# Performance work log

Measured on AMD Instinct MI355X. Metric: run time of the kernel, lower is better.

Reference implementation:

```python
import jax, jax.numpy as jnp
import numpy as np

T, G, K, N = 131072, 64, 1024, 512  # batch_sum, batch_count, k, n
M_MAX = 4096  # static upper bound on any group size (setup guarantees <= 3072)
PAD = 128     # tile alignment for padded offsets


def setup_inputs() -> dict:
    key = jax.random.key(0)
    k1, k2 = jax.random.split(key)
    a = jax.random.normal(k1, (T, K), dtype=jnp.float32)
    b = jax.random.normal(k2, (G, K, N), dtype=jnp.float32) / np.float32(np.sqrt(K))
    rng = np.random.default_rng(0)
    d = rng.integers(-1024, 1024, G // 2)
    deltas = np.concatenate([d, -d])
    rng.shuffle(deltas)
    sizes = (T // G) + deltas  # each in [1024, 3072], sums exactly to T
    offsets = np.concatenate([[0], np.cumsum(sizes)[:-1]])
    padded = ((sizes + PAD - 1) // PAD) * PAD
    padded_offsets = np.concatenate([[0], np.cumsum(padded)[:-1]])
    return {
        "a": a,
        "b": b,
        "batch_sizes": jnp.asarray(sizes, dtype=jnp.int32),
        "batch_offsets": jnp.asarray(offsets, dtype=jnp.int32),
        "batch_padded_offsets": jnp.asarray(padded_offsets, dtype=jnp.int32),
    }


def reference(a, b, batch_sizes, batch_offsets, batch_padded_offsets):
    # Grouped GEMM: for each group g, out[off_g : off_g+size_g] = a[rows] @ b[g].
    # jit-friendly: scan over groups with a fixed M_MAX window, mask invalid rows.
    T_, _ = a.shape
    n_out = b.shape[-1]
    iota = jnp.arange(M_MAX)

    def body(out, xs):
        off, size, bg = xs
        rows = jnp.clip(off + iota, 0, T_ - 1)          # [M_MAX]
        mask = iota < size                               # [M_MAX]
        a_g = jnp.where(mask[:, None], a[rows], 0.0)     # [M_MAX, K]
        y = a_g @ bg                                     # [M_MAX, N]
        out = out.at[rows].add(y)                        # masked rows add zeros
        return out, None

    out0 = jnp.zeros((T_, n_out), dtype=a.dtype)
    out, _ = jax.lax.scan(body, out0, (batch_offsets, batch_sizes, b))
    return out
```

## Files before the change

kernel.cpp:

```cpp
#include <hip/hip_runtime.h>
#include <hip/hip_bf16.h>
#include <stdint.h>

#define T_ROWS 131072
#define GCNT   64
#define KDIM   1024
#define NDIM   512
#define BM     256
#define BN     256
#define BK     64
#define KTILES (KDIM / BK)
#define MT_MAX 640
#define NBLK   (MT_MAX * 2)

typedef __attribute__((ext_vector_type(4))) float f32x4;
typedef __attribute__((ext_vector_type(8))) short s16x8;
typedef __attribute__((ext_vector_type(4))) short s16x4;
typedef __attribute__((address_space(3))) unsigned int lds_u32;
typedef const __attribute__((address_space(1))) unsigned int gbl_u32;

static __device__ __forceinline__ short f2bf(float f) {
  __hip_bfloat16 h = __float2bfloat16(f);
  return __builtin_bit_cast(short, h);
}

__global__ __launch_bounds__(256) void bt_kernel(const float* __restrict__ b,
                                                 char* __restrict__ bt) {
  __shared__ short lt[64 * 130];
  int bid = blockIdx.x;
  int kt = bid & 15, nt = (bid >> 4) & 3, g = bid >> 6;
  int t = threadIdx.x;
  const float* src = b + ((size_t)(g * KDIM + kt * BK)) * NDIM + nt * 128;
#pragma unroll
  for (int i = 0; i < 32; i++) {
    int idx = i * 256 + t;
    int kk = idx >> 7, nn = idx & 127;
    lt[kk * 130 + nn] = f2bf(src[(size_t)kk * NDIM + nn]);
  }
  __syncthreads();
  char* dst = bt + ((size_t)bid << 14);
#pragma unroll
  for (int j = 0; j < 4; j++) {
    int chunk = j * 256 + t;
    int n = chunk >> 3;
    int slot = (chunk & 7) ^ (n & 7);
    s16x8 v;
#pragma unroll
    for (int i = 0; i < 8; i++) v[i] = lt[(slot * 8 + i) * 130 + n];
    *(s16x8*)(dst + (size_t)chunk * 16) = v;
  }
}

template <bool USE_BT>
__global__ __launch_bounds__(512, 2) void gemm_kernel(
    const float* __restrict__ a, const float* __restrict__ b,
    const char* __restrict__ bt, const int* __restrict__ sizes,
    const int* __restrict__ offs, float* __restrict__ out) {
  __shared__ __align__(16) short lds_a[2][BM * BK];
  __shared__ __align__(16) char lds_b[2][BN * BK * 2];

  int bid0 = blockIdx.x;
  int bid = (bid0 & 7) * (NBLK / 8) + (bid0 >> 3);
  int bn = bid & 1;
  int tm = bid >> 1;

  int g = -1, m_loc = 0, base = 0;
#pragma unroll
  for (int i = 0; i < GCNT; i++) {
    int ps = (sizes[i] + 127) & ~127;
    int tg = (ps + 255) >> 8;
    if (tm >= base && tm < base + tg) { g = i; m_loc = (tm - base) << 8; }
    base += tg;
  }
  if (g < 0) return;
  int size = sizes[g];
  int off = offs[g];
  int valid = size - m_loc;

  int t = threadIdx.x;
  int lane = t & 63;
  int wid = t >> 6;
  int wm = wid >> 2, wn = wid & 3;
  int lr = lane & 15, q = lane >> 4;

  int r0 = t >> 4;
  int c16 = t & 15;
  int aoff[8];
#pragma unroll
  for (int i = 0; i < 8; i++) {
    int row = off + m_loc + i * 32 + r0;
    if (row >= T_ROWS) row = T_ROWS - 1;
    aoff[i] = row * KDIM + c16 * 4;
  }
  int a_wbyte = r0 * 128 + (((c16 >> 1) ^ (r0 & 7)) << 4) + (c16 & 1) * 8;

  int fb_n = t >> 1, fb_kh = (t & 1) * 32;

  const char* btbase = bt + (((size_t)g) << 20);

  f32x4 acc[8][4];
#pragma unroll
  for (int i = 0; i < 8; i++)
#pragma unroll
    for (int j = 0; j < 4; j++) acc[i][j] = (f32x4){0.f, 0.f, 0.f, 0.f};

  f32x4 va[8];

  auto loadA = [&](int kt) {
#pragma unroll
    for (int i = 0; i < 8; i++)
      va[i] = *(const f32x4*)(a + aoff[i] + kt * BK);
  };
  auto writeA = [&](int c) {
    char* db = (char*)lds_a[c] + a_wbyte;
#pragma unroll
    for (int i = 0; i < 8; i++) {
      s16x4 v;
#pragma unroll
      for (int e = 0; e < 4; e++) v[e] = f2bf(va[i][e]);
      *(s16x4*)(db + i * 4096) = v;
    }
  };
  auto stageB_bt = [&](int kt, int c) {
#pragma unroll
    for (int i = 0; i < 4; i++) {
      int wc = wid * 4 + i;
      int sub = wc >> 4;
      int cc = (wc & 15) * 64 + lane;
      const char* gsrc =
          btbase + (((size_t)((bn * 2 + sub) * 16 + kt)) << 14) + cc * 16;
      __builtin_amdgcn_global_load_lds(
          (gbl_u32*)gsrc, (lds_u32*)((char*)lds_b[c] + wc * 1024), 16, 0, 0);
    }
  };
  auto stageB_fb = [&](int kt, int c) {
    const float* p = b + (size_t)g * KDIM * NDIM +
                     (size_t)(kt * BK + fb_kh) * NDIM + bn * BN + fb_n;
    float vals[32];
#pragma unroll
    for (int i = 0; i < 32; i++) vals[i] = p[(size_t)i * NDIM];
    int nn = fb_n & 127;
    char* lb = (char*)lds_b[c] + (fb_n >> 7) * 16384 + nn * 128;
#pragma unroll
    for (int i8 = 0; i8 < 4; i8++) {
      int slot = (fb_kh >> 3) + i8;
      s16x8 v;
#pragma unroll
      for (int e = 0; e < 8; e++) v[e] = f2bf(vals[i8 * 8 + e]);
      *(s16x8*)(lb + (((slot ^ (nn & 7))) << 4)) = v;
    }
  };
  auto compute = [&](int c) {
    const char* As = (const char*)lds_a[c];
    const char* Bs = (const char*)lds_b[c];
#pragma unroll
    for (int ks = 0; ks < 2; ks++) {
      s16x8 af[8], bfr[4];
#pragma unroll
      for (int fm = 0; fm < 8; fm++) {
        int row = wm * 128 + fm * 16 + lr;
        int slot = (ks * 4 + q) ^ (row & 7);
        af[fm] = *(const s16x8*)(As + row * 128 + slot * 16);
      }
#pragma unroll
      for (int fn = 0; fn < 4; fn++) {
        int n = wn * 64 + fn * 16 + lr;
        int slot = (ks * 4 + q) ^ (n & 7);
        bfr[fn] = *(const s16x8*)(Bs + (n >> 7) * 16384 + (n & 127) * 128 +
                                  slot * 16);
      }
      __builtin_amdgcn_s_setprio(1);
#pragma unroll
      for (int fm = 0; fm < 8; fm++)
#pragma unroll
        for (int fn = 0; fn < 4; fn++)
          acc[fm][fn] = __builtin_amdgcn_mfma_f32_16x16x32_bf16(
              af[fm], bfr[fn], acc[fm][fn], 0, 0, 0);
      __builtin_amdgcn_s_setprio(0);
    }
  };

  loadA(0);
  if (USE_BT) stageB_bt(0, 0);
  else stageB_fb(0, 0);
  writeA(0);
  __syncthreads();

  int cur = 0;
  for (int kt = 0; kt < KTILES; kt++) {
    if (kt + 1 < KTILES) {
      loadA(kt + 1);
      if (USE_BT) stageB_bt(kt + 1, cur ^ 1);
    }
    compute(cur);
    if (kt + 1 < KTILES) {
      if (!USE_BT) stageB_fb(kt + 1, cur ^ 1);
      writeA(cur ^ 1);
      __syncthreads();
      cur ^= 1;
    }
  }

  size_t orow0 = (size_t)(off + m_loc);
#pragma unroll
  for (int fm = 0; fm < 8; fm++) {
#pragma unroll
    for (int j = 0; j < 4; j++) {
      int rm = wm * 128 + fm * 16 + q * 4 + j;
      if (rm < valid) {
        float* orow = out + (orow0 + rm) * NDIM + bn * BN + wn * 64 + lr;
#pragma unroll
        for (int fn = 0; fn < 4; fn++) orow[fn * 16] = acc[fm][fn][j];
      }
    }
  }
}

extern "C" void kernel_launch(void* const* d_in, const int* in_sizes, int n_in,
                              void* d_out, int out_size, void* d_ws,
                              size_t ws_size, hipStream_t stream) {
  const float* a = (const float*)d_in[0];
  const float* b = (const float*)d_in[1];
  const int* sizes = (const int*)d_in[2];
  const int* offs = (const int*)d_in[3];
  float* out = (float*)d_out;

  const size_t bt_bytes = (size_t)GCNT * KDIM * NDIM * 2;
  if (ws_size >= bt_bytes) {
    bt_kernel<<<GCNT * 64, 256, 0, stream>>>(b, (char*)d_ws);
    gemm_kernel<true><<<NBLK, 512, 0, stream>>>(a, b, (const char*)d_ws,
                                                sizes, offs, out);
  } else {
    gemm_kernel<false><<<NBLK, 512, 0, stream>>>(a, b, (const char*)nullptr,
                                                 sizes, offs, out);
  }
}
```

Before: 342.3 us.

## Split main loop into barrier-separated phases interleaving LDS reads, global loads and MFMA

Replaces the template GEMM's main loop in the workspace path with an 8-phase schedule. Each K tile is split into quarter MFMA blocks, with LDS fragment reads and halves of the next tile's A/B global loads issued between explicit s_barrier/sched_barrier pairs. The aim is to overlap memory traffic with matrix math and keep fewer fragments live in registers. In exchange it adds many workgroup barriers and a full vmcnt/lgkmcnt wait per tile, which may stall waves. The fallback path is split out as a separate kernel and loses its setprio calls.

```diff
diff --git a/kernel.cpp b/kernel.cpp
--- a/kernel.cpp
+++ b/kernel.cpp
@@ -51,11 +51,10 @@
   }
 }
 
-template <bool USE_BT>
-__global__ __launch_bounds__(512, 2) void gemm_kernel(
-    const float* __restrict__ a, const float* __restrict__ b,
-    const char* __restrict__ bt, const int* __restrict__ sizes,
-    const int* __restrict__ offs, float* __restrict__ out) {
+__global__ __launch_bounds__(512, 2) void gemm8(
+    const float* __restrict__ a, const char* __restrict__ bt,
+    const int* __restrict__ sizes, const int* __restrict__ offs,
+    float* __restrict__ out) {
   __shared__ __align__(16) short lds_a[2][BM * BK];
   __shared__ __align__(16) char lds_b[2][BN * BK * 2];
 
@@ -73,18 +72,12 @@
     base += tg;
   }
   if (g < 0) return;
-  int size = sizes[g];
-  int off = offs[g];
-  int valid = size - m_loc;
-
-  int t = threadIdx.x;
-  int lane = t & 63;
-  int wid = t >> 6;
-  int wm = wid >> 2, wn = wid & 3;
-  int lr = lane & 15, q = lane >> 4;
-
-  int r0 = t >> 4;
-  int c16 = t & 15;
+  int size = sizes[g], off = offs[g], valid = size - m_loc;
+
+  int t = threadIdx.x, lane = t & 63, wid = t >> 6;
+  int wm = wid >> 2, wn = wid & 3, lr = lane & 15, q = lane >> 4;
+
+  int r0 = t >> 4, c16 = t & 15;
   int aoff[8];
 #pragma unroll
   for (int i = 0; i < 8; i++) {
@@ -94,37 +87,25 @@
   }
   int a_wbyte = r0 * 128 + (((c16 >> 1) ^ (r0 & 7)) << 4) + (c16 & 1) * 8;
 
-  int fb_n = t >> 1, fb_kh = (t & 1) * 32;
-
-  const char* btbase = bt + (((size_t)g) << 20);
+  const char* btbase = bt + ((size_t)g << 20);
 
   f32x4 acc[8][4];
 #pragma unroll
   for (int i = 0; i < 8; i++)
 #pragma unroll
     for (int j = 0; j < 4; j++) acc[i][j] = (f32x4){0.f, 0.f, 0.f, 0.f};
-
   f32x4 va[8];
-
-  auto loadA = [&](int kt) {
-#pragma unroll
-    for (int i = 0; i < 8; i++)
-      va[i] = *(const f32x4*)(a + aoff[i] + kt * BK);
-  };
-  auto writeA = [&](int c) {
-    char* db = (char*)lds_a[c] + a_wbyte;
-#pragma unroll
-    for (int i = 0; i < 8; i++) {
-      s16x4 v;
-#pragma unroll
-      for (int e = 0; e < 4; e++) v[e] = f2bf(va[i][e]);
-      *(s16x4*)(db + i * 4096) = v;
-    }
-  };
-  auto stageB_bt = [&](int kt, int c) {
-#pragma unroll
-    for (int i = 0; i < 4; i++) {
-      int wc = wid * 4 + i;
+  s16x8 af[4], bf0[4], bf1[4];
+
+  auto issueA = [&](int kt, int h) {
+#pragma unroll
+    for (int i = 0; i < 4; i++)
+      va[h * 4 + i] = *(const f32x4*)(a + aoff[h * 4 + i] + kt * BK);
+  };
+  auto issueB = [&](int kt, int c, int h) {
+#pragma unroll
+    for (int i = 0; i < 2; i++) {
+      int wc = wid * 4 + h * 2 + i;
       int sub = wc >> 4;
       int cc = (wc & 15) * 64 + lane;
       const char* gsrc =
@@ -133,7 +114,162 @@
           (gbl_u32*)gsrc, (lds_u32*)((char*)lds_b[c] + wc * 1024), 16, 0, 0);
     }
   };
-  auto stageB_fb = [&](int kt, int c) {
+  auto writeA = [&](int c) {
+    char* db = (char*)lds_a[c] + a_wbyte;
+#pragma unroll
+    for (int i = 0; i < 8; i++) {
+      s16x4 v;
+#pragma unroll
+      for (int e = 0; e < 4; e++) v[e] = f2bf(va[i][e]);
+      *(s16x4*)(db + i * 4096) = v;
+    }
+  };
+  auto dsA = [&](int c, int half, int ks) {
+#pragma unroll
+    for (int i = 0; i < 4; i++) {
+      int row = wm * 128 + (half * 4 + i) * 16 + lr;
+      int slot = (ks * 4 + q) ^ (row & 7);
+      af[i] = *(const s16x8*)((const char*)lds_a[c] + row * 128 + slot * 16);
+    }
+  };
+  auto dsB = [&](int c, int ks, s16x8* bf) {
+#pragma unroll
+    for (int fn = 0; fn < 4; fn++) {
+      int n = wn * 64 + fn * 16 + lr;
+      int slot = (ks * 4 + q) ^ (n & 7);
+      bf[fn] = *(const s16x8*)((const char*)lds_b[c] + (n >> 7) * 16384 +
+                               (n & 127) * 128 + slot * 16);
+    }
+  };
+  auto bar = [&]() {
+    __builtin_amdgcn_s_barrier();
+    __builtin_amdgcn_sched_barrier(0);
+  };
+  auto mfmaQ = [&](const s16x8* bf, int fmb) {
+    __builtin_amdgcn_s_setprio(1);
+#pragma unroll
+    for (int fm = 0; fm < 4; fm++)
+#pragma unroll
+      for (int fn = 0; fn < 4; fn++)
+        acc[fmb + fm][fn] = __builtin_amdgcn_mfma_f32_16x16x32_bf16(
+            af[fm], bf[fn], acc[fmb + fm][fn], 0, 0, 0);
+    __builtin_amdgcn_s_setprio(0);
+  };
+
+  issueA(0, 0);
+  issueA(0, 1);
+  issueB(0, 0, 0);
+  issueB(0, 0, 1);
+  writeA(0);
+  asm volatile("s_waitcnt vmcnt(0) lgkmcnt(0)" ::: "memory");
+  bar();
+
+  for (int kt = 0; kt < KTILES; kt++) {
+    int cur = kt & 1, nxt = cur ^ 1;
+    bool more = (kt + 1 < KTILES);
+    dsA(cur, 0, 0);
+    dsB(cur, 0, bf0);
+    if (more) issueA(kt + 1, 0);
+    bar();
+    mfmaQ(bf0, 0);
+    bar();
+    dsA(cur, 0, 1);
+    dsB(cur, 1, bf1);
+    if (more) issueA(kt + 1, 1);
+    bar();
+    mfmaQ(bf1, 0);
+    bar();
+    dsA(cur, 1, 0);
+    if (more) issueB(kt + 1, nxt, 0);
+    bar();
+    mfmaQ(bf0, 4);
+    bar();
+    dsA(cur, 1, 1);
+    if (more) issueB(kt + 1, nxt, 1);
+    bar();
+    mfmaQ(bf1, 4);
+    bar();
+    if (more) {
+      writeA(nxt);
+      asm volatile("s_waitcnt vmcnt(0) lgkmcnt(0)" ::: "memory");
+      bar();
+    }
+  }
+
+  size_t orow0 = (size_t)(off + m_loc);
+#pragma unroll
+  for (int fm = 0; fm < 8; fm++) {
+#pragma unroll
+    for (int j = 0; j < 4; j++) {
+      int rm = wm * 128 + fm * 16 + q * 4 + j;
+      if (rm < valid) {
+        float* orow = out + (orow0 + rm) * NDIM + bn * BN + wn * 64 + lr;
+#pragma unroll
+        for (int fn = 0; fn < 4; fn++) orow[fn * 16] = acc[fm][fn][j];
+      }
+    }
+  }
+}
+
+__global__ __launch_bounds__(512, 2) void gemm_fb(
+    const float* __restrict__ a, const float* __restrict__ b,
+    const int* __restrict__ sizes, const int* __restrict__ offs,
+    float* __restrict__ out) {
+  __shared__ __align__(16) short lds_a[2][BM * BK];
+  __shared__ __align__(16) char lds_b[2][BN * BK * 2];
+
+  int bid0 = blockIdx.x;
+  int bid = (bid0 & 7) * (NBLK / 8) + (bid0 >> 3);
+  int bn = bid & 1;
+  int tm = bid >> 1;
+
+  int g = -1, m_loc = 0, base = 0;
+#pragma unroll
+  for (int i = 0; i < GCNT; i++) {
+    int ps = (sizes[i] + 127) & ~127;
+    int tg = (ps + 255) >> 8;
+    if (tm >= base && tm < base + tg) { g = i; m_loc = (tm - base) << 8; }
+    base += tg;
+  }
+  if (g < 0) return;
+  int size = sizes[g], off = offs[g], valid = size - m_loc;
+
+  int t = threadIdx.x, lane = t & 63, wid = t >> 6;
+  int wm = wid >> 2, wn = wid & 3, lr = lane & 15, q = lane >> 4;
+
+  int r0 = t >> 4, c16 = t & 15;
+  int aoff[8];
+#pragma unroll
+  for (int i = 0; i < 8; i++) {
+    int row = off + m_loc + i * 32 + r0;
+    if (row >= T_ROWS) row = T_ROWS - 1;
+    aoff[i] = row * KDIM + c16 * 4;
+  }
+  int a_wbyte = r0 * 128 + (((c16 >> 1) ^ (r0 & 7)) << 4) + (c16 & 1) * 8;
+  int fb_n = t >> 1, fb_kh = (t & 1) * 32;
+
+  f32x4 acc[8][4];
+#pragma unroll
+  for (int i = 0; i < 8; i++)
+#pragma unroll
+    for (int j = 0; j < 4; j++) acc[i][j] = (f32x4){0.f, 0.f, 0.f, 0.f};
+  f32x4 va[8];
+
+  auto loadA = [&](int kt) {
+#pragma unroll
+    for (int i = 0; i < 8; i++) va[i] = *(const f32x4*)(a + aoff[i] + kt * BK);
+  };
+  auto writeA = [&](int c) {
+    char* db = (char*)lds_a[c] + a_wbyte;
+#pragma unroll
+    for (int i = 0; i < 8; i++) {
+      s16x4 v;
+#pragma unroll
+      for (int e = 0; e < 4; e++) v[e] = f2bf(va[i][e]);
+      *(s16x4*)(db + i * 4096) = v;
+    }
+  };
+  auto stageB = [&](int kt, int c) {
     const float* p = b + (size_t)g * KDIM * NDIM +
                      (size_t)(kt * BK + fb_kh) * NDIM + bn * BN + fb_n;
     float vals[32];
@@ -151,8 +287,6 @@
     }
   };
   auto compute = [&](int c) {
-    const char* As = (const char*)lds_a[c];
-    const char* Bs = (const char*)lds_b[c];
 #pragma unroll
     for (int ks = 0; ks < 2; ks++) {
       s16x8 af[8], bfr[4];
@@ -160,47 +294,39 @@
       for (int fm = 0; fm < 8; fm++) {
         int row = wm * 128 + fm * 16 + lr;
         int slot = (ks * 4 + q) ^ (row & 7);
-        af[fm] = *(const s16x8*)(As + row * 128 + slot * 16);
+        af[fm] = *(const s16x8*)((const char*)lds_a[c] + row * 128 + slot * 16);
       }
 #pragma unroll
       for (int fn = 0; fn < 4; fn++) {
         int n = wn * 64 + fn * 16 + lr;
         int slot = (ks * 4 + q) ^ (n & 7);
-        bfr[fn] = *(const s16x8*)(Bs + (n >> 7) * 16384 + (n & 127) * 128 +
-                                  slot * 16);
+        bfr[fn] = *(const s16x8*)((const char*)lds_b[c] + (n >> 7) * 16384 +
+                                  (n & 127) * 128 + slot * 16);
       }
-      __builtin_amdgcn_s_setprio(1);
 #pragma unroll
       for (int fm = 0; fm < 8; fm++)
 #pragma unroll
         for (int fn = 0; fn < 4; fn++)
           acc[fm][fn] = __builtin_amdgcn_mfma_f32_16x16x32_bf16(
               af[fm], bfr[fn], acc[fm][fn], 0, 0, 0);
-      __builtin_amdgcn_s_setprio(0);
     }
   };
 
   loadA(0);
-  if (USE_BT) stageB_bt(0, 0);
-  else stageB_fb(0, 0);
+  stageB(0, 0);
   writeA(0);
   __syncthreads();
-
   int cur = 0;
   for (int kt = 0; kt < KTILES; kt++) {
-    if (kt + 1 < KTILES) {
-      loadA(kt + 1);
-      if (USE_BT) stageB_bt(kt + 1, cur ^ 1);
-    }
+    if (kt + 1 < KTILES) loadA(kt + 1);
     compute(cur);
     if (kt + 1 < KTILES) {
-      if (!USE_BT) stageB_fb(kt + 1, cur ^ 1);
+      stageB(kt + 1, cur ^ 1);
       writeA(cur ^ 1);
       __syncthreads();
       cur ^= 1;
     }
   }
-
   size_t orow0 = (size_t)(off + m_loc);
 #pragma unroll
   for (int fm = 0; fm < 8; fm++) {
@@ -228,10 +354,8 @@
   const size_t bt_bytes = (size_t)GCNT * KDIM * NDIM * 2;
   if (ws_size >= bt_bytes) {
     bt_kernel<<<GCNT * 64, 256, 0, stream>>>(b, (char*)d_ws);
-    gemm_kernel<true><<<NBLK, 512, 0, stream>>>(a, b, (const char*)d_ws,
-                                                sizes, offs, out);
+    gemm8<<<NBLK, 512, 0, stream>>>(a, (const char*)d_ws, sizes, offs, out);
   } else {
-    gemm_kernel<false><<<NBLK, 512, 0, stream>>>(a, b, (const char*)nullptr,
-                                                 sizes, offs, out);
-  }
-}
+    gemm_fb<<<NBLK, 512, 0, stream>>>(a, b, sizes, offs, out);
+  }
+}
```

Result: faster. 307.5 us (-10.2%).
